# Performance work log

Measured on AMD Instinct MI355X. Metric: run time of the kernel, lower is better.

Reference implementation:

```python
import jax, jax.numpy as jnp
import numpy as np

N = 50000    # num genes (nodes)
E = 500000   # edges per edge type
T = 2        # edge types
L = 2        # gnn layers
H = 4        # attention heads
D = 64       # per-head channels (hidden // heads)
HID = 256    # hidden channels
PRE_IN = 1024
OUT = 64
EPS = 1e-5
SLOPE = 0.2  # PyG GATv2 leaky_relu negative slope


def _layer_norm(x, g, b):
    mu = x.mean(-1, keepdims=True)
    v = x.var(-1, keepdims=True)
    return (x - mu) / jnp.sqrt(v + EPS) * g + b


def _seg_softmax(score, seg, n):
    m = jax.ops.segment_max(score, seg, num_segments=n)
    ex = jnp.exp(score - m[seg])
    den = jax.ops.segment_sum(ex, seg, num_segments=n)
    return ex / (den[seg] + 1e-16)


def _gatv2_projected(x, src, dst, Wl, Wr, att, bias, Wp, bp):
    # GATv2Conv (share_weights=False, concat heads) followed by Linear projection
    n = x.shape[0]
    xl = (x @ Wl).reshape(n, H, D)
    xr = (x @ Wr).reshape(n, H, D)
    hs = xl[src]                                   # [E,H,D] messages from source
    e = jax.nn.leaky_relu(hs + xr[dst], SLOPE)     # [E,H,D]
    score = jnp.einsum('ehd,hd->eh', e, att)       # [E,H]
    alpha = _seg_softmax(score, dst, n)            # softmax over in-edges of dst
    out = jax.ops.segment_sum(hs * alpha[:, :, None], dst, num_segments=n)
    out = out.reshape(n, H * D) + bias             # concat heads + conv bias
    return out @ Wp + bp                           # ProjectedGATConv linear


def setup_inputs() -> dict:
    key = jax.random.key(0)
    ks = jax.random.split(key, 20)
    s = 0.05
    return {
        'x': jax.random.normal(ks[0], (N, PRE_IN), dtype=jnp.float32),
        'edge_index_0': jax.random.randint(ks[1], (2, E), 0, N, dtype=jnp.int32),
        'edge_index_1': jax.random.randint(ks[2], (2, E), 0, N, dtype=jnp.int32),
        'pre_W0': jax.random.normal(ks[3], (PRE_IN, HID)) * s,
        'pre_b0': jnp.zeros((HID,)),
        'pre_g0': jnp.ones((HID,)),
        'pre_be0': jnp.zeros((HID,)),
        'pre_W1': jax.random.normal(ks[4], (HID, HID)) * s,
        'pre_b1': jnp.zeros((HID,)),
        'pre_g1': jnp.ones((HID,)),
        'pre_be1': jnp.zeros((HID,)),
        # HeteroGnn: L layers x T edge types of ProjectedGATConv(GATv2)
        'gat_Wl': jax.random.normal(ks[5], (L, T, HID, H * D)) * s,
        'gat_Wr': jax.random.normal(ks[6], (L, T, HID, H * D)) * s,
        'gat_att': jax.random.normal(ks[7], (L, T, H, D)) * 0.1,
        'gat_bias': jnp.zeros((L, T, H * D)),
        'proj_W': jax.random.normal(ks[8], (L, T, H * D, HID)) * s,
        'proj_b': jnp.zeros((L, T, HID)),
        # prediction head: Linear(HID,HID) + relu + Linear(HID,OUT)
        'head_W0': jax.random.normal(ks[9], (HID, HID)) * s,
        'head_b0': jnp.zeros((HID,)),
        'head_W1': jax.random.normal(ks[10], (HID, OUT)) * s,
        'head_b1': jnp.zeros((OUT,)),
    }


def reference(x, edge_index_0, edge_index_1, pre_W0, pre_b0, pre_g0, pre_be0,
              pre_W1, pre_b1, pre_g1, pre_be1, gat_Wl, gat_Wr, gat_att,
              gat_bias, proj_W, proj_b, head_W0, head_b0, head_W1, head_b1):
    loop = jnp.arange(N, dtype=edge_index_0.dtype)  # add_self_loops=True
    edges = [(jnp.concatenate([ei[0], loop]), jnp.concatenate([ei[1], loop]))
             for ei in (edge_index_0, edge_index_1)]
    # preprocessor MLP
    h = jax.nn.relu(_layer_norm(x @ pre_W0 + pre_b0, pre_g0, pre_be0))
    h = jax.nn.relu(_layer_norm(h @ pre_W1 + pre_b1, pre_g1, pre_be1))
    # hetero GAT stack, HeteroConv aggr='sum'
    for l in range(L):
        acc = jnp.zeros((N, HID), dtype=h.dtype)
        for t in range(T):
            src, dst = edges[t]
            acc = acc + _gatv2_projected(h, src, dst, gat_Wl[l, t], gat_Wr[l, t],
                                         gat_att[l, t], gat_bias[l, t],
                                         proj_W[l, t], proj_b[l, t])
        h = jax.nn.relu(acc)
    # prediction head
    h2 = jax.nn.relu(h @ head_W0 + head_b0)
    return h2 @ head_W1 + head_b1
```

## Files before the change

### kernel.cpp

```cpp
#include <hip/hip_runtime.h>
#include <hip/hip_bf16.h>
#include <math.h>

#define N_NODES 50000
#define MP      50048
#define E_EDGES 500000
#define EPRIME  (E_EDGES + N_NODES)
#define HID     256
#define PRE_IN  1024
#define OUT_DIM 64
#define NHEAD   4
#define DHEAD   64
#define LAYERS  2
#define NTYPES  2

#define SCAN_NBLK 49
#define NPAD      (SCAN_NBLK * 1024)

typedef __attribute__((ext_vector_type(8))) short short8v;
typedef __attribute__((ext_vector_type(4))) float f32x4;
typedef _Float16 h2v __attribute__((ext_vector_type(2)));
typedef _Float16 h8v __attribute__((ext_vector_type(8)));

__device__ __forceinline__ ushort f2bf(float f) {
  uint u = __float_as_uint(f);
  u += 0x7FFF + ((u >> 16) & 1);
  return (ushort)(u >> 16);
}
__device__ __forceinline__ float bf2f(ushort u) {
  return __uint_as_float(((uint)u) << 16);
}

#define WAITV3 asm volatile("s_waitcnt vmcnt(3)" ::: "memory")
#define WAITV0 asm volatile("s_waitcnt vmcnt(0)" ::: "memory")
#define WAITLG asm volatile("s_waitcnt lgkmcnt(0)" ::: "memory")
#define SCHEDB __builtin_amdgcn_sched_barrier(0)
#define BARRIER __builtin_amdgcn_s_barrier()

template<bool AF32>
__global__ __launch_bounds__(256) void gemm_k(
    const void* __restrict__ Ap,
    const ushort* __restrict__ Bt,
    int K, int M, int N,
    float*  __restrict__ Cf,
    ushort* __restrict__ Cb,
    const float* __restrict__ bias,
    const float* __restrict__ bias2,
    int do_relu, int out_f16)
{
  __shared__ ushort As[3][128 * 32];
  __shared__ ushort Bs[3][64 * 32];
  const int tid = threadIdx.x;
  const int l   = tid & 63;
  const int w   = tid >> 6;
  const int wm  = w & 1;
  const int wn  = w >> 1;

  const int nwg  = gridDim.x * gridDim.y;
  const int orig = blockIdx.y * gridDim.x + blockIdx.x;
  const int qq   = nwg >> 3, rr = nwg & 7;
  const int xcd  = orig & 7;
  const int wgid = ((xcd < rr) ? xcd * (qq + 1) : rr * (qq + 1) + (xcd - rr) * qq)
                   + (orig >> 3);
  const int bm = (wgid / gridDim.x) * 128;
  const int bn = (wgid % gridDim.x) * 64;

  f32x4 acc[4][2];
#pragma unroll
  for (int m = 0; m < 4; m++)
#pragma unroll
    for (int n = 0; n < 2; n++) acc[m][n] = (f32x4){0.f, 0.f, 0.f, 0.f};

  const int srow  = l >> 2;
  const int sslot = l & 3;
  const int nt    = K >> 5;

  int  arow[2], akc[2];
  uint aoff[2];
#pragma unroll
  for (int i = 0; i < 2; i++) {
    arow[i] = w * 32 + i * 16 + srow;
    akc[i]  = sslot ^ ((arow[i] >> 1) & 3);
    aoff[i] = (uint)arow[i] * 64 + (uint)sslot * 16;
  }
  const int brow  = tid >> 2;
  const int bslot = tid & 3;
  const int bkc   = bslot ^ ((brow >> 1) & 3);

  float4 pf[2][2];
  if constexpr (AF32) {
#pragma unroll
    for (int i = 0; i < 2; i++) {
      pf[i][0] = make_float4(0.f, 0.f, 0.f, 0.f);
      pf[i][1] = make_float4(0.f, 0.f, 0.f, 0.f);
    }
  }

#define STAGE_B(t, buf)                                                        \
  {                                                                            \
    const ushort* gb = Bt + (size_t)(bn + brow) * K + ((t) << 5) + bkc * 8;    \
    __builtin_amdgcn_global_load_lds(                                          \
        (const __attribute__((address_space(1))) uint*)gb,                     \
        (__attribute__((address_space(3))) uint*)((char*)Bs[buf] + tid * 16),  \
        16, 0, 0);                                                             \
  }
#define STAGE_A16(t, buf)                                                      \
  _Pragma("unroll")                                                            \
  for (int i = 0; i < 2; i++) {                                                \
    const ushort* ga = (const ushort*)Ap + (size_t)(bm + arow[i]) * K +        \
                       ((t) << 5) + akc[i] * 8;                                \
    __builtin_amdgcn_global_load_lds(                                          \
        (const __attribute__((address_space(1))) uint*)ga,                     \
        (__attribute__((address_space(3))) uint*)((char*)As[buf] + aoff[i]),   \
        16, 0, 0);                                                             \
  }
#define LOAD_A32(t)                                                            \
  _Pragma("unroll")                                                            \
  for (int i = 0; i < 2; i++) {                                                \
    if (bm + arow[i] < M) {                                                    \
      const float* ga = (const float*)Ap + (size_t)(bm + arow[i]) * K +        \
                        ((t) << 5) + akc[i] * 8;                               \
      pf[i][0] = *reinterpret_cast<const float4*>(ga);                         \
      pf[i][1] = *reinterpret_cast<const float4*>(ga + 4);                     \
    }                                                                          \
  }
#define WRITE_A32(buf)                                                         \
  _Pragma("unroll")                                                            \
  for (int i = 0; i < 2; i++) {                                                \
    short8v s;                                                                 \
    s[0] = (short)f2bf(pf[i][0].x); s[1] = (short)f2bf(pf[i][0].y);            \
    s[2] = (short)f2bf(pf[i][0].z); s[3] = (short)f2bf(pf[i][0].w);            \
    s[4] = (short)f2bf(pf[i][1].x); s[5] = (short)f2bf(pf[i][1].y);            \
    s[6] = (short)f2bf(pf[i][1].z); s[7] = (short)f2bf(pf[i][1].w);            \
    *reinterpret_cast<short8v*>((char*)As[buf] + aoff[i]) = s;                 \
  }

  if constexpr (AF32) {
    STAGE_B(0, 0);
    LOAD_A32(0);
    WRITE_A32(0);
    STAGE_B(1, 1);
    LOAD_A32(1);
    WAITLG; SCHEDB; BARRIER; SCHEDB;
  } else {
    STAGE_B(0, 0); STAGE_A16(0, 0);
    STAGE_B(1, 1); STAGE_A16(1, 1);
    WAITV3;
    SCHEDB; BARRIER; SCHEDB;
  }

  int rd = 0;
  for (int t = 0; t < nt; t++) {
    int wr = rd + 1; if (wr == 3) wr = 0;
    int st = wr + 1; if (st == 3) st = 0;

    if constexpr (AF32) {
      if (t + 1 < nt) WRITE_A32(wr);
      if (t + 2 < nt) { STAGE_B(t + 2, st); LOAD_A32(t + 2); }
    } else {
      if (t + 2 < nt) { STAGE_B(t + 2, st); STAGE_A16(t + 2, st); }
    }

    short8v a[4], b[2];
#pragma unroll
    for (int m = 0; m < 4; m++) {
      const int row = wm * 64 + m * 16 + (l & 15);
      const int kc  = (l >> 4) ^ ((row >> 1) & 3);
      a[m] = *(const short8v*)((const char*)As[rd] + row * 64 + kc * 16);
    }
#pragma unroll
    for (int n = 0; n < 2; n++) {
      const int row = wn * 32 + n * 16 + (l & 15);
      const int kc  = (l >> 4) ^ ((row >> 1) & 3);
      b[n] = *(const short8v*)((const char*)Bs[rd] + row * 64 + kc * 16);
    }
#pragma unroll
    for (int m = 0; m < 4; m++)
#pragma unroll
      for (int n = 0; n < 2; n++)
        acc[m][n] = __builtin_amdgcn_mfma_f32_16x16x32_bf16(a[m], b[n], acc[m][n], 0, 0, 0);

    if (t + 1 < nt) {
      if constexpr (AF32) {
        WAITLG;
      } else {
        if (t + 2 < nt) { WAITV3; }
        else            { WAITV0; }
      }
      SCHEDB; BARRIER; SCHEDB;
    }
    rd = wr;
  }

  const int crow0 = bm + wm * 64 + (l >> 4) * 4;
  const int ccol0 = bn + wn * 32 + (l & 15);
#pragma unroll
  for (int m = 0; m < 4; m++) {
#pragma unroll
    for (int j = 0; j < 4; j++) {
      const int grow = crow0 + m * 16 + j;
      if (grow < M) {
#pragma unroll
        for (int n = 0; n < 2; n++) {
          const int gcol = ccol0 + n * 16;
          if (gcol < N) {
            float v = acc[m][n][j];
            if (bias)  v += bias[gcol];
            if (bias2) v += bias2[gcol];
            if (do_relu) v = fmaxf(v, 0.f);
            if (Cf) Cf[(size_t)grow * N + gcol] = v;
            else if (out_f16) {
              _Float16 hv = (_Float16)v;
              Cb[(size_t)grow * N + gcol] = *(ushort*)&hv;
            } else {
              Cb[(size_t)grow * N + gcol] = f2bf(v);
            }
          }
        }
      }
    }
  }
}

__global__ void ln_relu(const float* __restrict__ in, ushort* __restrict__ out,
                        const float* __restrict__ g, const float* __restrict__ be, int n)
{
  int gid = blockIdx.x * blockDim.x + threadIdx.x;
  int row = gid >> 6;
  int lane = threadIdx.x & 63;
  if (row >= n) return;
  float4 v = *reinterpret_cast<const float4*>(in + (size_t)row * HID + lane * 4);
  float s = v.x + v.y + v.z + v.w;
  float ss = v.x * v.x + v.y * v.y + v.z * v.z + v.w * v.w;
#pragma unroll
  for (int o = 1; o < 64; o <<= 1) { s += __shfl_xor(s, o); ss += __shfl_xor(ss, o); }
  float mu = s * (1.f / 256.f);
  float var = ss * (1.f / 256.f) - mu * mu;
  float inv = rsqrtf(var + 1e-5f);
  float4 gg = *reinterpret_cast<const float4*>(g + lane * 4);
  float4 bb = *reinterpret_cast<const float4*>(be + lane * 4);
  ushort4 o4;
  o4.x = f2bf(fmaxf((v.x - mu) * inv * gg.x + bb.x, 0.f));
  o4.y = f2bf(fmaxf((v.y - mu) * inv * gg.y + bb.y, 0.f));
  o4.z = f2bf(fmaxf((v.z - mu) * inv * gg.z + bb.z, 0.f));
  o4.w = f2bf(fmaxf((v.w - mu) * inv * gg.w + bb.w, 0.f));
  *reinterpret_cast<ushort4*>(out + (size_t)row * HID + lane * 4) = o4;
}

__global__ void csr_count2(const int* __restrict__ ei0, const int* __restrict__ ei1,
                           int* __restrict__ cnt0, int* __restrict__ cnt1)
{
  int e = blockIdx.x * blockDim.x + threadIdx.x;
  if (e >= 2 * EPRIME) return;
  int type = e >= EPRIME;
  int i = type ? e - EPRIME : e;
  const int* ei = type ? ei1 : ei0;
  int* cnt = type ? cnt1 : cnt0;
  int d = (i < E_EDGES) ? ei[E_EDGES + i] : (i - E_EDGES);
  atomicAdd(&cnt[d], 1);
}

__global__ __launch_bounds__(256) void scan_p1(const int* __restrict__ cnt0,
                                               const int* __restrict__ cnt1,
                                               int* __restrict__ bsums)
{
  int type = blockIdx.x >= SCAN_NBLK;
  int blk = type ? blockIdx.x - SCAN_NBLK : blockIdx.x;
  const int* cnt = type ? cnt1 : cnt0;
  int4 v = reinterpret_cast<const int4*>(cnt)[blk * 256 + threadIdx.x];
  int s = v.x + v.y + v.z + v.w;
#pragma unroll
  for (int o = 1; o < 64; o <<= 1) s += __shfl_xor(s, o);
  __shared__ int wt[4];
  if ((threadIdx.x & 63) == 0) wt[threadIdx.x >> 6] = s;
  __syncthreads();
  if (threadIdx.x == 0) bsums[blockIdx.x] = wt[0] + wt[1] + wt[2] + wt[3];
}

__global__ void scan_p2(const int* __restrict__ bsums, int* __restrict__ boffs,
                        int* __restrict__ offs0, int* __restrict__ offs1)
{
  int t = threadIdx.x;
  if (t < 2) {
    int run = 0;
    for (int i = 0; i < SCAN_NBLK; i++) {
      boffs[t * SCAN_NBLK + i] = run;
      run += bsums[t * SCAN_NBLK + i];
    }
  }
  if (t == 2) offs0[N_NODES] = EPRIME;
  if (t == 3) offs1[N_NODES] = EPRIME;
}

__global__ __launch_bounds__(256) void scan_p3(
    const int* __restrict__ cnt0, const int* __restrict__ cnt1,
    const int* __restrict__ boffs,
    int* __restrict__ offs0, int* __restrict__ cur0,
    int* __restrict__ offs1, int* __restrict__ cur1)
{
  int type = blockIdx.x >= SCAN_NBLK;
  int blk = type ? blockIdx.x - SCAN_NBLK : blockIdx.x;
  const int* cnt = type ? cnt1 : cnt0;
  int* offs = type ? offs1 : offs0;
  int* cur  = type ? cur1 : cur0;
  const int tid = threadIdx.x, lane = tid & 63, wv = tid >> 6;
  int4 v = reinterpret_cast<const int4*>(cnt)[blk * 256 + tid];
  int e1 = v.x, e2 = e1 + v.y, e3 = e2 + v.z, T = e3 + v.w;
  int incl = T;
#pragma unroll
  for (int o = 1; o < 64; o <<= 1) {
    int nb = __shfl_up(incl, o);
    if (lane >= o) incl += nb;
  }
  __shared__ int wt[4];
  if (lane == 63) wt[wv] = incl;
  __syncthreads();
  int wexcl = 0;
  for (int i = 0; i < wv; i++) wexcl += wt[i];
  int base = boffs[blockIdx.x] + wexcl + (incl - T);
  int idx = blk * 1024 + tid * 4;
  int4 o4 = make_int4(base, base + e1, base + e2, base + e3);
  if (idx + 3 < N_NODES) {
    reinterpret_cast<int4*>(offs)[idx >> 2] = o4;
    reinterpret_cast<int4*>(cur)[idx >> 2] = o4;
  } else {
    if (idx + 0 < N_NODES) { offs[idx + 0] = o4.x; cur[idx + 0] = o4.x; }
    if (idx + 1 < N_NODES) { offs[idx + 1] = o4.y; cur[idx + 1] = o4.y; }
    if (idx + 2 < N_NODES) { offs[idx + 2] = o4.z; cur[idx + 2] = o4.z; }
    if (idx + 3 < N_NODES) { offs[idx + 3] = o4.w; cur[idx + 3] = o4.w; }
  }
}

__global__ void csr_scatter2(const int* __restrict__ ei0, const int* __restrict__ ei1,
                             int* __restrict__ cur0, int* __restrict__ cur1,
                             int* __restrict__ csr0, int* __restrict__ csr1)
{
  int e = blockIdx.x * blockDim.x + threadIdx.x;
  if (e >= 2 * EPRIME) return;
  int type = e >= EPRIME;
  int i = type ? e - EPRIME : e;
  const int* ei = type ? ei1 : ei0;
  int* cur = type ? cur1 : cur0;
  int* csr = type ? csr1 : csr0;
  int d = (i < E_EDGES) ? ei[E_EDGES + i] : (i - E_EDGES);
  int s = (i < E_EDGES) ? ei[i] : (i - E_EDGES);
  int pos = atomicAdd(&cur[d], 1);
  csr[pos] = s;
}

__global__ void csr_sort2(const int* __restrict__ offs0, int* __restrict__ csr0,
                          const int* __restrict__ offs1, int* __restrict__ csr1)
{
  int d = blockIdx.x * blockDim.x + threadIdx.x;
  if (d >= 2 * N_NODES) return;
  int type = d >= N_NODES;
  int i = type ? d - N_NODES : d;
  const int* offs = type ? offs1 : offs0;
  int* csr = type ? csr1 : csr0;
  int b = offs[i], e = offs[i + 1];
  for (int p = b + 1; p < e; p++) {
    int v = csr[p];
    int j = p - 1;
    while (j >= b && csr[j] > v) { csr[j + 1] = csr[j]; j--; }
    csr[j + 1] = v;
  }
}

#define WSEG0 262144
#define WSEG1 (WSEG0 + 65536)
#define WSEG2 (WSEG1 + 524288)
#define WSEG3 (WSEG2 + 262144)
#define WSEG4 (WSEG3 + 65536)
#define WSEG5 (WSEG4 + 32768)
__global__ void wtrans_all(const float* __restrict__ pre_W0, const float* __restrict__ pre_W1,
                           const float* __restrict__ Wl, const float* __restrict__ Wr,
                           const float* __restrict__ proj_W,
                           const float* __restrict__ head_W0, const float* __restrict__ head_W1,
                           ushort* __restrict__ W0t, ushort* __restrict__ W1t,
                           ushort* __restrict__ WcatT, ushort* __restrict__ projcatT,
                           ushort* __restrict__ hW0t, ushort* __restrict__ hW1t)
{
  int i = blockIdx.x * blockDim.x + threadIdx.x;
  if (i < WSEG0) {
    int nrow = i >> 10, k = i & 1023;
    W0t[i] = f2bf(pre_W0[(size_t)k * 256 + nrow]);
  } else if (i < WSEG1) {
    int j = i - WSEG0;
    int nrow = j >> 8, k = j & 255;
    W1t[j] = f2bf(pre_W1[(size_t)k * 256 + nrow]);
  } else if (i < WSEG2) {
    int j = i - WSEG1;
    int l = j >> 18;
    int rem = j & 262143;
    int c = rem >> 8, k = rem & 255;
    int t = c >> 9, half = (c >> 8) & 1, cc = c & 255;
    const float* W = half ? Wr : Wl;
    WcatT[j] = f2bf(W[(((size_t)l * NTYPES + t) * 256 + k) * 256 + cc]);
  } else if (i < WSEG3) {
    int j = i - WSEG2;
    int l = j >> 17;
    int rem = j & 131071;
    int n = rem >> 9, k = rem & 511;
    int t = k >> 8, kk = k & 255;
    projcatT[j] = f2bf(proj_W[(((size_t)l * NTYPES + t) * 256 + kk) * 256 + n]);
  } else if (i < WSEG4) {
    int j = i - WSEG3;
    int nrow = j >> 8, k = j & 255;
    hW0t[j] = f2bf(head_W0[(size_t)k * 256 + nrow]);
  } else if (i < WSEG5) {
    int j = i - WSEG4;
    int nrow = j >> 8, k = j & 255;
    hW1t[j] = (nrow < OUT_DIM) ? f2bf(head_W1[(size_t)k * OUT_DIM + nrow]) : (ushort)0;
  }
}

__device__ __forceinline__ float dpp8_sum(float p) {
  p += __int_as_float(__builtin_amdgcn_update_dpp(0, __float_as_int(p), 0xB1, 0xF, 0xF, true));
  p += __int_as_float(__builtin_amdgcn_update_dpp(0, __float_as_int(p), 0x4E, 0xF, 0xF, true));
  p += __int_as_float(__builtin_amdgcn_update_dpp(0, __float_as_int(p), 0x141, 0xF, 0xF, true));
  return p;
}

__device__ __forceinline__ h8v leaky8(h8v x) {
  const _Float16 c = (_Float16)0.2f;
  h8v y = x * c;
#if __has_builtin(__builtin_elementwise_max)
  return __builtin_elementwise_max(x, y);
#else
  h8v r;
#pragma unroll
  for (int i = 0; i < 8; i++) r[i] = x[i] > y[i] ? x[i] : y[i];
  return r;
#endif
}

__device__ __forceinline__ float dot8(h8v e, const h2v* a) {
  h2v e0 = {e[0], e[1]}, e1 = {e[2], e[3]}, e2 = {e[4], e[5]}, e3 = {e[6], e[7]};
#if __has_builtin(__builtin_amdgcn_fdot2)
  float s = __builtin_amdgcn_fdot2(e0, a[0], 0.f, false);
  s = __builtin_amdgcn_fdot2(e1, a[1], s, false);
  s = __builtin_amdgcn_fdot2(e2, a[2], s, false);
  s = __builtin_amdgcn_fdot2(e3, a[3], s, false);
  return s;
#else
  float s = 0.f;
#pragma unroll
  for (int i = 0; i < 8; i++) s += (float)e[i] * (float)a[i >> 1][i & 1];
  return s;
#endif
}

__global__ __launch_bounds__(256) void gat_edge3(
    const _Float16* __restrict__ xlr,
    const int* __restrict__ offs0, const int* __restrict__ csr0,
    const int* __restrict__ offs1, const int* __restrict__ csr1,
    const float* __restrict__ att,
    const float* __restrict__ bias,
    ushort* __restrict__ out, int nblk_per_type)
{
  const int type = blockIdx.x >= nblk_per_type;
  const int bid = type ? blockIdx.x - nblk_per_type : blockIdx.x;
  const int wid = (bid * 256 + threadIdx.x) >> 6;
  if (wid >= N_NODES) return;
  const int lane = threadIdx.x & 63;
  const int half = lane >> 5, li = lane & 31;
  const int* offs = type ? offs1 : offs0;
  const int* csr  = type ? csr1 : csr0;
  const int xl_col = type ? 512 : 0;

  const float* ap = att + type * 256 + li * 8;
  h2v a[4];
#pragma unroll
  for (int i = 0; i < 4; i++) {
    a[i][0] = (_Float16)ap[2 * i];
    a[i][1] = (_Float16)ap[2 * i + 1];
  }
  const h8v xr = *reinterpret_cast<const h8v*>(xlr + (size_t)wid * 1024 + xl_col + 256 + li * 8);

  const int beg = offs[wid], end = offs[wid + 1];
  const float L2E = 1.44269504f;
  float m = -1e30f, den = 0.f;
  float acc[8];
#pragma unroll
  for (int i = 0; i < 8; i++) acc[i] = 0.f;

  const int ng = (end - beg + 3) >> 2;
  for (int g = 0; g < ng; g++) {
    const int j0 = beg + 4 * g + half;
    const int j1 = j0 + 2;
    const bool v0 = j0 < end, v1 = j1 < end;
    const int s0 = csr[v0 ? j0 : beg];
    const int s1 = csr[v1 ? j1 : beg];
    const h8v hs0 = *reinterpret_cast<const h8v*>(xlr + (size_t)s0 * 1024 + xl_col + li * 8);
    const h8v hs1 = *reinterpret_cast<const h8v*>(xlr + (size_t)s1 * 1024 + xl_col + li * 8);
    float p0 = dpp8_sum(dot8(leaky8(hs0 + xr), a));
    float p1 = dpp8_sum(dot8(leaky8(hs1 + xr), a));
    if (!v0) p0 = -INFINITY;
    if (!v1) p1 = -INFINITY;
    const float pm = fmaxf(p0, p1);
    if (__any(pm > m + 4.f)) {
      const float nm = fmaxf(m, pm);
      const float so = exp2f((m - nm) * L2E);
      den *= so;
#pragma unroll
      for (int i = 0; i < 8; i++) acc[i] *= so;
      m = nm;
    }
    const float w0 = exp2f((p0 - m) * L2E);
    const float w1 = exp2f((p1 - m) * L2E);
    den += w0 + w1;
#pragma unroll
    for (int i = 0; i < 8; i++) {
      acc[i] = fmaf((float)hs0[i], w0, acc[i]);
      acc[i] = fmaf((float)hs1[i], w1, acc[i]);
    }
  }

  const float mo  = __shfl_xor(m, 32);
  const float dno = __shfl_xor(den, 32);
  const float ms = fmaxf(m, mo);
  const float fa = exp2f((m - ms) * L2E);
  const float fb = exp2f((mo - ms) * L2E);
  const float r = 1.f / (den * fa + dno * fb + 1e-16f);
  float of[8];
#pragma unroll
  for (int i = 0; i < 8; i++)
    of[i] = (acc[i] * fa + __shfl_xor(acc[i], 32) * fb) * r;

  if (half == 0) {
    const float* bp = bias + type * 256 + li * 8;
    uint4 o;
    uint pk[4];
#pragma unroll
    for (int i = 0; i < 4; i++) {
      const uint lo = f2bf(of[2 * i] + bp[2 * i]);
      const uint hi = f2bf(of[2 * i + 1] + bp[2 * i + 1]);
      pk[i] = lo | (hi << 16);
    }
    o.x = pk[0]; o.y = pk[1]; o.z = pk[2]; o.w = pk[3];
    *reinterpret_cast<uint4*>(out + (size_t)wid * 512 + type * 256 + li * 8) = o;
  }
}

extern "C" void kernel_launch(void* const* d_in, const int* in_sizes, int n_in,
                              void* d_out, int out_size, void* d_ws, size_t ws_size,
                              hipStream_t stream)
{
  const float* x        = (const float*)d_in[0];
  const int*   ei0      = (const int*)d_in[1];
  const int*   ei1      = (const int*)d_in[2];
  const float* pre_W0   = (const float*)d_in[3];
  const float* pre_b0   = (const float*)d_in[4];
  const float* pre_g0   = (const float*)d_in[5];
  const float* pre_be0  = (const float*)d_in[6];
  const float* pre_W1   = (const float*)d_in[7];
  const float* pre_b1   = (const float*)d_in[8];
  const float* pre_g1   = (const float*)d_in[9];
  const float* pre_be1  = (const float*)d_in[10];
  const float* gat_Wl   = (const float*)d_in[11];
  const float* gat_Wr   = (const float*)d_in[12];
  const float* gat_att  = (const float*)d_in[13];
  const float* gat_bias = (const float*)d_in[14];
  const float* proj_W   = (const float*)d_in[15];
  const float* proj_b   = (const float*)d_in[16];
  const float* head_W0  = (const float*)d_in[17];
  const float* head_b0  = (const float*)d_in[18];
  const float* head_W1  = (const float*)d_in[19];
  const float* head_b1  = (const float*)d_in[20];
  float* outp = (float*)d_out;

  char* ws = (char*)d_ws;
  ushort* xlr_b = (ushort*)ws; ws += (size_t)MP * 1024 * 2;
  ushort* hb    = (ushort*)ws; ws += (size_t)MP * 256 * 2;
  ushort* outt  = (ushort*)ws; ws += (size_t)MP * 512 * 2;
  float*  tmp   = (float*)outt;
  ushort* hbuf  = (ushort*)outt;
  ushort* W0t      = (ushort*)ws; ws += (size_t)256 * 1024 * 2;
  ushort* W1t      = (ushort*)ws; ws += (size_t)256 * 256 * 2;
  ushort* WcatT    = (ushort*)ws; ws += (size_t)LAYERS * 1024 * 256 * 2;
  ushort* projcatT = (ushort*)ws; ws += (size_t)LAYERS * 256 * 512 * 2;
  ushort* hW0t     = (ushort*)ws; ws += (size_t)256 * 256 * 2;
  ushort* hW1t     = (ushort*)ws; ws += (size_t)128 * 256 * 2;
  int* cnt0  = (int*)ws; ws += (size_t)NPAD * 4;
  int* cnt1  = (int*)ws; ws += (size_t)NPAD * 4;
  int* offs0 = (int*)ws; ws += (size_t)(N_NODES + 4) * 4;
  int* offs1 = (int*)ws; ws += (size_t)(N_NODES + 4) * 4;
  int* cur0  = (int*)ws; ws += (size_t)N_NODES * 4;
  int* cur1  = (int*)ws; ws += (size_t)N_NODES * 4;
  int* bsums = (int*)ws; ws += (size_t)128 * 4;
  int* boffs = (int*)ws; ws += (size_t)128 * 4;
  int* csr0  = (int*)ws; ws += (size_t)EPRIME * 4;
  int* csr1  = (int*)ws; ws += (size_t)EPRIME * 4;

  hipMemsetAsync(cnt0, 0, (size_t)2 * NPAD * 4, stream);
  const int gE2 = (2 * EPRIME + 255) / 256;
  csr_count2<<<gE2, 256, 0, stream>>>(ei0, ei1, cnt0, cnt1);
  scan_p1<<<2 * SCAN_NBLK, 256, 0, stream>>>(cnt0, cnt1, bsums);
  scan_p2<<<1, 64, 0, stream>>>(bsums, boffs, offs0, offs1);
  scan_p3<<<2 * SCAN_NBLK, 256, 0, stream>>>(cnt0, cnt1, boffs, offs0, cur0, offs1, cur1);
  csr_scatter2<<<gE2, 256, 0, stream>>>(ei0, ei1, cur0, cur1, csr0, csr1);
  csr_sort2<<<(2 * N_NODES + 255) / 256, 256, 0, stream>>>(offs0, csr0, offs1, csr1);

  wtrans_all<<<WSEG5 / 256, 256, 0, stream>>>(pre_W0, pre_W1, gat_Wl, gat_Wr, proj_W,
                                              head_W0, head_W1,
                                              W0t, W1t, WcatT, projcatT, hW0t, hW1t);

  const dim3 blk(256);
  const int gy = MP / 128;
  const int gln = (N_NODES * 64 + 255) / 256;

  gemm_k<true><<<dim3(4, gy), blk, 0, stream>>>(x, W0t, 1024, N_NODES, 256,
                                                tmp, nullptr, pre_b0, nullptr, 0, 0);
  ln_relu<<<gln, 256, 0, stream>>>(tmp, hb, pre_g0, pre_be0, N_NODES);
  gemm_k<false><<<dim3(4, gy), blk, 0, stream>>>(hb, W1t, 256, N_NODES, 256,
                                                 tmp, nullptr, pre_b1, nullptr, 0, 0);
  ln_relu<<<gln, 256, 0, stream>>>(tmp, hb, pre_g1, pre_be1, N_NODES);

  for (int l = 0; l < LAYERS; l++) {
    gemm_k<false><<<dim3(16, gy), blk, 0, stream>>>(hb, WcatT + (size_t)l * 1024 * 256,
                                                    256, N_NODES, 1024,
                                                    nullptr, xlr_b, nullptr, nullptr, 0, 1);
    gat_edge3<<<2 * gln, 256, 0, stream>>>(
        (const _Float16*)xlr_b, offs0, csr0, offs1, csr1,
        gat_att  + (size_t)l * NTYPES * NHEAD * DHEAD,
        gat_bias + (size_t)l * NTYPES * HID,
        outt, gln);
    gemm_k<false><<<dim3(4, gy), blk, 0, stream>>>(
        outt, projcatT + (size_t)l * 256 * 512, 512, N_NODES, 256,
        nullptr, hb,
        proj_b + (size_t)(l * NTYPES + 0) * HID,
        proj_b + (size_t)(l * NTYPES + 1) * HID, 1, 0);
  }

  gemm_k<false><<<dim3(4, gy), blk, 0, stream>>>(hb, hW0t, 256, N_NODES, 256,
                                                 nullptr, hbuf, head_b0, nullptr, 1, 0);
  gemm_k<false><<<dim3(1, gy), blk, 0, stream>>>(hbuf, hW1t, 256, N_NODES, OUT_DIM,
                                                 outp, nullptr, head_b1, nullptr, 0, 0);
}
```

Before: 816.4 us.

## Split-K preprocessor GEMMs and replace triple-buffered pipeline with single-buffer sync loop

The GEMM kernel gains a split-K mode: a z grid dimension selects a K slice and a second fp32 output, and the LayerNorm kernel adds the two partials. This doubles the number of workgroups for the two preprocessor GEMMs. The kernel also drops its 3-stage LDS ring buffer and hand-tuned waitcnt pipeline in favour of a single buffer with a __syncthreads around every K tile. That removes load/compute overlap in every GEMM, including the large per-layer ones, and risks exposing memory latency.

```diff
diff --git a/kernel.cpp b/kernel.cpp
--- a/kernel.cpp
+++ b/kernel.cpp
@@ -31,9 +31,6 @@
   return __uint_as_float(((uint)u) << 16);
 }
 
-#define WAITV3 asm volatile("s_waitcnt vmcnt(3)" ::: "memory")
-#define WAITV0 asm volatile("s_waitcnt vmcnt(0)" ::: "memory")
-#define WAITLG asm volatile("s_waitcnt lgkmcnt(0)" ::: "memory")
 #define SCHEDB __builtin_amdgcn_sched_barrier(0)
 #define BARRIER __builtin_amdgcn_s_barrier()
 
@@ -41,29 +38,36 @@
 __global__ __launch_bounds__(256) void gemm_k(
     const void* __restrict__ Ap,
     const ushort* __restrict__ Bt,
-    int K, int M, int N,
+    int lda, int Klen, int M, int N,
     float*  __restrict__ Cf,
+    float*  __restrict__ Cfz,
     ushort* __restrict__ Cb,
     const float* __restrict__ bias,
     const float* __restrict__ bias2,
     int do_relu, int out_f16)
 {
-  __shared__ ushort As[3][128 * 32];
-  __shared__ ushort Bs[3][64 * 32];
+  __shared__ ushort As[128 * 32];
+  __shared__ ushort Bs[64 * 32];
   const int tid = threadIdx.x;
   const int l   = tid & 63;
   const int w   = tid >> 6;
   const int wm  = w & 1;
   const int wn  = w >> 1;
 
-  const int nwg  = gridDim.x * gridDim.y;
-  const int orig = blockIdx.y * gridDim.x + blockIdx.x;
+  const int gx = gridDim.x, gyy = gridDim.y;
+  const int nwg  = gx * gyy * gridDim.z;
+  const int orig = (blockIdx.z * gyy + blockIdx.y) * gx + blockIdx.x;
   const int qq   = nwg >> 3, rr = nwg & 7;
   const int xcd  = orig & 7;
   const int wgid = ((xcd < rr) ? xcd * (qq + 1) : rr * (qq + 1) + (xcd - rr) * qq)
                    + (orig >> 3);
-  const int bm = (wgid / gridDim.x) * 128;
-  const int bn = (wgid % gridDim.x) * 64;
+  const int px = wgid % gx;
+  const int py = (wgid / gx) % gyy;
+  const int pz = wgid / (gx * gyy);
+  const int bm = py * 128;
+  const int bn = px * 64;
+  const int koff = pz * Klen;
+  float* const outF = pz ? Cfz : Cf;
 
   f32x4 acc[4][2];
 #pragma unroll
@@ -73,7 +77,7 @@
 
   const int srow  = l >> 2;
   const int sslot = l & 3;
-  const int nt    = K >> 5;
+  const int nt    = Klen >> 5;
 
   int  arow[2], akc[2];
   uint aoff[2];
@@ -87,44 +91,36 @@
   const int bslot = tid & 3;
   const int bkc   = bslot ^ ((brow >> 1) & 3);
 
-  float4 pf[2][2];
-  if constexpr (AF32) {
-#pragma unroll
-    for (int i = 0; i < 2; i++) {
-      pf[i][0] = make_float4(0.f, 0.f, 0.f, 0.f);
-      pf[i][1] = make_float4(0.f, 0.f, 0.f, 0.f);
-    }
-  }
-
-#define STAGE_B(t, buf)                                                        \
+#define STAGE_B(t)                                                             \
   {                                                                            \
-    const ushort* gb = Bt + (size_t)(bn + brow) * K + ((t) << 5) + bkc * 8;    \
+    const ushort* gb = Bt + (size_t)(bn + brow) * lda + koff + ((t) << 5) +    \
+                       bkc * 8;                                                \
     __builtin_amdgcn_global_load_lds(                                          \
         (const __attribute__((address_space(1))) uint*)gb,                     \
-        (__attribute__((address_space(3))) uint*)((char*)Bs[buf] + tid * 16),  \
+        (__attribute__((address_space(3))) uint*)((char*)Bs + tid * 16),       \
         16, 0, 0);                                                             \
   }
-#define STAGE_A16(t, buf)                                                      \
+#define STAGE_A16(t)                                                           \
   _Pragma("unroll")                                                            \
   for (int i = 0; i < 2; i++) {                                                \
-    const ushort* ga = (const ushort*)Ap + (size_t)(bm + arow[i]) * K +        \
-                       ((t) << 5) + akc[i] * 8;                                \
+    const ushort* ga = (const ushort*)Ap + (size_t)(bm + arow[i]) * lda +      \
+                       koff + ((t) << 5) + akc[i] * 8;                         \
     __builtin_amdgcn_global_load_lds(                                          \
         (const __attribute__((address_space(1))) uint*)ga,                     \
-        (__attribute__((address_space(3))) uint*)((char*)As[buf] + aoff[i]),   \
+        (__attribute__((address_space(3))) uint*)((char*)As + aoff[i]),        \
         16, 0, 0);                                                             \
   }
 #define LOAD_A32(t)                                                            \
   _Pragma("unroll")                                                            \
   for (int i = 0; i < 2; i++) {                                                \
     if (bm + arow[i] < M) {                                                    \
-      const float* ga = (const float*)Ap + (size_t)(bm + arow[i]) * K +        \
-                        ((t) << 5) + akc[i] * 8;                               \
+      const float* ga = (const float*)Ap + (size_t)(bm + arow[i]) * lda +      \
+                        koff + ((t) << 5) + akc[i] * 8;                        \
       pf[i][0] = *reinterpret_cast<const float4*>(ga);                         \
       pf[i][1] = *reinterpret_cast<const float4*>(ga + 4);                     \
     }                                                                          \
   }
-#define WRITE_A32(buf)                                                         \
+#define WRITE_A32()                                                            \
   _Pragma("unroll")                                                            \
   for (int i = 0; i < 2; i++) {                                                \
     short8v s;                                                                 \
@@ -132,64 +128,64 @@
     s[2] = (short)f2bf(pf[i][0].z); s[3] = (short)f2bf(pf[i][0].w);            \
     s[4] = (short)f2bf(pf[i][1].x); s[5] = (short)f2bf(pf[i][1].y);            \
     s[6] = (short)f2bf(pf[i][1].z); s[7] = (short)f2bf(pf[i][1].w);            \
-    *reinterpret_cast<short8v*>((char*)As[buf] + aoff[i]) = s;                 \
+    *reinterpret_cast<short8v*>((char*)As + aoff[i]) = s;                      \
+  }
+#define COMPUTE_TILE()                                                         \
+  {                                                                            \
+    short8v a[4], b[2];                                                        \
+    _Pragma("unroll")                                                          \
+    for (int m = 0; m < 4; m++) {                                              \
+      const int row = wm * 64 + m * 16 + (l & 15);                             \
+      const int kc  = (l >> 4) ^ ((row >> 1) & 3);                             \
+      a[m] = *(const short8v*)((const char*)As + row * 64 + kc * 16);          \
+    }                                                                          \
+    _Pragma("unroll")                                                          \
+    for (int n = 0; n < 2; n++) {                                              \
+      const int row = wn * 32 + n * 16 + (l & 15);                             \
+      const int kc  = (l >> 4) ^ ((row >> 1) & 3);                             \
+      b[n] = *(const short8v*)((const char*)Bs + row * 64 + kc * 16);          \
+    }                                                                          \
+    _Pragma("unroll")                                                          \
+    for (int m = 0; m < 4; m++)                                                \
+      _Pragma("unroll")                                                        \
+      for (int n = 0; n < 2; n++)                                              \
+        acc[m][n] = __builtin_amdgcn_mfma_f32_16x16x32_bf16(a[m], b[n],        \
+                                                            acc[m][n], 0, 0, 0);\
   }
 
   if constexpr (AF32) {
-    STAGE_B(0, 0);
+    float4 pf[2][2];
+#pragma unroll
+    for (int i = 0; i < 2; i++) {
+      pf[i][0] = make_float4(0.f, 0.f, 0.f, 0.f);
+      pf[i][1] = make_float4(0.f, 0.f, 0.f, 0.f);
+    }
     LOAD_A32(0);
-    WRITE_A32(0);
-    STAGE_B(1, 1);
-    LOAD_A32(1);
-    WAITLG; SCHEDB; BARRIER; SCHEDB;
+    STAGE_B(0);
+    WRITE_A32();
+    asm volatile("s_waitcnt vmcnt(0) lgkmcnt(0)" ::: "memory");
+    SCHEDB; BARRIER; SCHEDB;
+    if (nt > 1) LOAD_A32(1);
+    for (int t = 0; t < nt; t++) {
+      COMPUTE_TILE();
+      if (t + 1 < nt) {
+        asm volatile("s_waitcnt lgkmcnt(0)" ::: "memory");
+        SCHEDB; BARRIER; SCHEDB;
+        STAGE_B(t + 1);
+        WRITE_A32();
+        asm volatile("s_waitcnt vmcnt(0) lgkmcnt(0)" ::: "memory");
+        SCHEDB; BARRIER; SCHEDB;
+        if (t + 2 < nt) LOAD_A32(t + 2);
+      }
+    }
   } else {
-    STAGE_B(0, 0); STAGE_A16(0, 0);
-    STAGE_B(1, 1); STAGE_A16(1, 1);
-    WAITV3;
-    SCHEDB; BARRIER; SCHEDB;
-  }
-
-  int rd = 0;
-  for (int t = 0; t < nt; t++) {
-    int wr = rd + 1; if (wr == 3) wr = 0;
-    int st = wr + 1; if (st == 3) st = 0;
-
-    if constexpr (AF32) {
-      if (t + 1 < nt) WRITE_A32(wr);
-      if (t + 2 < nt) { STAGE_B(t + 2, st); LOAD_A32(t + 2); }
-    } else {
-      if (t + 2 < nt) { STAGE_B(t + 2, st); STAGE_A16(t + 2, st); }
-    }
-
-    short8v a[4], b[2];
-#pragma unroll
-    for (int m = 0; m < 4; m++) {
-      const int row = wm * 64 + m * 16 + (l & 15);
-      const int kc  = (l >> 4) ^ ((row >> 1) & 3);
-      a[m] = *(const short8v*)((const char*)As[rd] + row * 64 + kc * 16);
-    }
-#pragma unroll
-    for (int n = 0; n < 2; n++) {
-      const int row = wn * 32 + n * 16 + (l & 15);
-      const int kc  = (l >> 4) ^ ((row >> 1) & 3);
-      b[n] = *(const short8v*)((const char*)Bs[rd] + row * 64 + kc * 16);
-    }
-#pragma unroll
-    for (int m = 0; m < 4; m++)
-#pragma unroll
-      for (int n = 0; n < 2; n++)
-        acc[m][n] = __builtin_amdgcn_mfma_f32_16x16x32_bf16(a[m], b[n], acc[m][n], 0, 0, 0);
-
-    if (t + 1 < nt) {
-      if constexpr (AF32) {
-        WAITLG;
-      } else {
-        if (t + 2 < nt) { WAITV3; }
-        else            { WAITV0; }
-      }
-      SCHEDB; BARRIER; SCHEDB;
-    }
-    rd = wr;
+    for (int t = 0; t < nt; t++) {
+      STAGE_B(t);
+      STAGE_A16(t);
+      __syncthreads();
+      COMPUTE_TILE();
+      __syncthreads();
+    }
   }
 
   const int crow0 = bm + wm * 64 + (l >> 4) * 4;
@@ -205,10 +201,12 @@
           const int gcol = ccol0 + n * 16;
           if (gcol < N) {
             float v = acc[m][n][j];
-            if (bias)  v += bias[gcol];
-            if (bias2) v += bias2[gcol];
+            if (pz == 0) {
+              if (bias)  v += bias[gcol];
+              if (bias2) v += bias2[gcol];
+            }
             if (do_relu) v = fmaxf(v, 0.f);
-            if (Cf) Cf[(size_t)grow * N + gcol] = v;
+            if (outF) outF[(size_t)grow * N + gcol] = v;
             else if (out_f16) {
               _Float16 hv = (_Float16)v;
               Cb[(size_t)grow * N + gcol] = *(ushort*)&hv;
@@ -222,7 +220,8 @@
   }
 }
 
-__global__ void ln_relu(const float* __restrict__ in, ushort* __restrict__ out,
+__global__ void ln_relu(const float* __restrict__ in, const float* __restrict__ in2,
+                        ushort* __restrict__ out,
                         const float* __restrict__ g, const float* __restrict__ be, int n)
 {
   int gid = blockIdx.x * blockDim.x + threadIdx.x;
@@ -230,6 +229,10 @@
   int lane = threadIdx.x & 63;
   if (row >= n) return;
   float4 v = *reinterpret_cast<const float4*>(in + (size_t)row * HID + lane * 4);
+  if (in2) {
+    float4 v2 = *reinterpret_cast<const float4*>(in2 + (size_t)row * HID + lane * 4);
+    v.x += v2.x; v.y += v2.y; v.z += v2.z; v.w += v2.w;
+  }
   float s = v.x + v.y + v.z + v.w;
   float ss = v.x * v.x + v.y * v.y + v.z * v.z + v.w * v.w;
 #pragma unroll
@@ -574,6 +577,7 @@
   ushort* hb    = (ushort*)ws; ws += (size_t)MP * 256 * 2;
   ushort* outt  = (ushort*)ws; ws += (size_t)MP * 512 * 2;
   float*  tmp   = (float*)outt;
+  float*  tmp2  = (float*)xlr_b;
   ushort* hbuf  = (ushort*)outt;
   ushort* W0t      = (ushort*)ws; ws += (size_t)256 * 1024 * 2;
   ushort* W1t      = (ushort*)ws; ws += (size_t)256 * 256 * 2;
@@ -609,31 +613,34 @@
   const int gy = MP / 128;
   const int gln = (N_NODES * 64 + 255) / 256;
 
-  gemm_k<true><<<dim3(4, gy), blk, 0, stream>>>(x, W0t, 1024, N_NODES, 256,
-                                                tmp, nullptr, pre_b0, nullptr, 0, 0);
-  ln_relu<<<gln, 256, 0, stream>>>(tmp, hb, pre_g0, pre_be0, N_NODES);
-  gemm_k<false><<<dim3(4, gy), blk, 0, stream>>>(hb, W1t, 256, N_NODES, 256,
-                                                 tmp, nullptr, pre_b1, nullptr, 0, 0);
-  ln_relu<<<gln, 256, 0, stream>>>(tmp, hb, pre_g1, pre_be1, N_NODES);
+  gemm_k<true><<<dim3(4, gy, 2), blk, 0, stream>>>(x, W0t, 1024, 512, N_NODES, 256,
+                                                   tmp, tmp2, nullptr, pre_b0, nullptr, 0, 0);
+  ln_relu<<<gln, 256, 0, stream>>>(tmp, tmp2, hb, pre_g0, pre_be0, N_NODES);
+  gemm_k<false><<<dim3(4, gy, 2), blk, 0, stream>>>(hb, W1t, 256, 128, N_NODES, 256,
+                                                    tmp, tmp2, nullptr, pre_b1, nullptr, 0, 0);
+  ln_relu<<<gln, 256, 0, stream>>>(tmp, tmp2, hb, pre_g1, pre_be1, N_NODES);
 
   for (int l = 0; l < LAYERS; l++) {
     gemm_k<false><<<dim3(16, gy), blk, 0, stream>>>(hb, WcatT + (size_t)l * 1024 * 256,
-                                                    256, N_NODES, 1024,
-                                                    nullptr, xlr_b, nullptr, nullptr, 0, 1);
+                                                    256, 256, N_NODES, 1024,
+                                                    nullptr, nullptr, xlr_b,
+                                                    nullptr, nullptr, 0, 1);
     gat_edge3<<<2 * gln, 256, 0, stream>>>(
         (const _Float16*)xlr_b, offs0, csr0, offs1, csr1,
         gat_att  + (size_t)l * NTYPES * NHEAD * DHEAD,
         gat_bias + (size_t)l * NTYPES * HID,
         outt, gln);
     gemm_k<false><<<dim3(4, gy), blk, 0, stream>>>(
-        outt, projcatT + (size_t)l * 256 * 512, 512, N_NODES, 256,
-        nullptr, hb,
+        outt, projcatT + (size_t)l * 256 * 512, 512, 512, N_NODES, 256,
+        nullptr, nullptr, hb,
         proj_b + (size_t)(l * NTYPES + 0) * HID,
         proj_b + (size_t)(l * NTYPES + 1) * HID, 1, 0);
   }
 
-  gemm_k<false><<<dim3(4, gy), blk, 0, stream>>>(hb, hW0t, 256, N_NODES, 256,
-                                                 nullptr, hbuf, head_b0, nullptr, 1, 0);
-  gemm_k<false><<<dim3(1, gy), blk, 0, stream>>>(hbuf, hW1t, 256, N_NODES, OUT_DIM,
-                                                 outp, nullptr, head_b1, nullptr, 0, 0);
-}
+  gemm_k<false><<<dim3(4, gy), blk, 0, stream>>>(hb, hW0t, 256, 256, N_NODES, 256,
+                                                 nullptr, nullptr, hbuf,
+                                                 head_b0, nullptr, 1, 0);
+  gemm_k<false><<<dim3(1, gy), blk, 0, stream>>>(hbuf, hW1t, 256, 256, N_NODES, OUT_DIM,
+                                                 outp, nullptr, nullptr,
+                                                 head_b1, nullptr, 0, 0);
+}
```

Result: no change. 805.3 us (-1.4%).
